# Kernel optimization log

Measured on AMD Instinct MI355X. Metric: run time of the kernel, lower is better.

Reference implementation:

```python
import jax, jax.numpy as jnp
import numpy as np

EPS = 1e-5

def layer_norm(h, g, b):
    mu = h.mean(axis=-1, keepdims=True)
    var = jnp.mean((h - mu) ** 2, axis=-1, keepdims=True)
    return (h - mu) * jax.lax.rsqrt(var + EPS) * g + b

def setup_inputs() -> dict:
    key = jax.random.key(0)
    B, J, D, Ae, A, H, EH, LAT = 32, 16384, 32, 16, 4096, 128, 256, 32
    ks = jax.random.split(key, 12)
    in_dim = 1 + D + Ae  # 49
    inp = {
        "x": jax.random.normal(ks[0], (B, J), dtype=jnp.float32),
        "mask": jax.random.randint(ks[1], (B, J), 0, 2, dtype=jnp.int32),
        "atse_index": jax.random.randint(ks[2], (J,), 0, A, dtype=jnp.int32),
        "feature_embedding": jax.random.normal(ks[3], (J, D), dtype=jnp.float32),
        "atse_embedding": jax.random.normal(ks[4], (A, Ae), dtype=jnp.float32),
        # h_layer: Linear(in_dim->H) + LN + ReLU + Linear(H->D) + LN + ReLU
        "hW1": jax.random.normal(ks[5], (in_dim, H), dtype=jnp.float32) / np.sqrt(in_dim),
        "hb1": jnp.zeros((H,), jnp.float32),
        "hg1": jnp.ones((H,), jnp.float32),
        "hB1": jnp.zeros((H,), jnp.float32),
        "hW2": jax.random.normal(ks[6], (H, D), dtype=jnp.float32) / np.sqrt(H),
        "hb2": jnp.zeros((D,), jnp.float32),
        "hg2": jnp.ones((D,), jnp.float32),
        "hB2": jnp.zeros((D,), jnp.float32),
        # encoder_mlp (FCLayers, 2 layers, LayerNorm + ReLU each): D->EH->2*LAT
        "eW1": jax.random.normal(ks[7], (D, EH), dtype=jnp.float32) / np.sqrt(D),
        "eb1": jnp.zeros((EH,), jnp.float32),
        "eg1": jnp.ones((EH,), jnp.float32),
        "eB1": jnp.zeros((EH,), jnp.float32),
        "eW2": jax.random.normal(ks[8], (EH, 2 * LAT), dtype=jnp.float32) / np.sqrt(EH),
        "eb2": jnp.zeros((2 * LAT,), jnp.float32),
        "eg2": jnp.ones((2 * LAT,), jnp.float32),
        "eB2": jnp.zeros((2 * LAT,), jnp.float32),
    }
    return inp

def reference(x, mask, atse_index, feature_embedding, atse_embedding,
              hW1, hb1, hg1, hB1, hW2, hb2, hg2, hB2,
              eW1, eb1, eg1, eB1, eW2, eb2, eg2, eB2):
    B, J = x.shape
    Ae_per_j = atse_embedding[atse_index]  # [J, Ae] gather
    # h_in per (b, j): [psi | F_j | E_atse(j)] -> [B, J, 1+D+Ae]
    h_in = jnp.concatenate([
        x[:, :, None],
        jnp.broadcast_to(feature_embedding[None], (B,) + feature_embedding.shape),
        jnp.broadcast_to(Ae_per_j[None], (B,) + Ae_per_j.shape),
    ], axis=-1)
    h = jax.nn.relu(layer_norm(h_in @ hW1 + hb1, hg1, hB1))   # [B, J, H]
    h = jax.nn.relu(layer_norm(h @ hW2 + hb2, hg2, hB2))      # [B, J, D]
    m = mask.astype(h.dtype)                                   # [B, J]
    pooled = jnp.einsum('bj,bjd->bd', m, h)                    # masked sum pool
    cnt = m.sum(axis=-1, keepdims=True)
    c = pooled / jnp.maximum(cnt, 1.0)                         # mean; zero rows stay zero
    e = jax.nn.relu(layer_norm(c @ eW1 + eb1, eg1, eB1))
    ml = jax.nn.relu(layer_norm(e @ eW2 + eb2, eg2, eB2))      # [B, 2*latent]
    mu, logvar = jnp.split(ml, 2, axis=-1)
    return mu, logvar
```

## Files before the change

kernel.cpp:

```cpp
#include <hip/hip_runtime.h>
#include <hip/hip_bf16.h>

#define JTOT  16384
#define BATCH 32
#define DD    32
#define AE    16
#define HH    128
#define EHD   256
#define LATD  32
#define NBLK  512
#define EPSV  1e-5f

typedef __attribute__((ext_vector_type(8))) short short8;
typedef __attribute__((ext_vector_type(4))) float f32x4;

#define OFF_BASE 0
#define OFF_XS   4224
#define OFF_MS   5280
#define OFF_W0   6336
#define OFF_G1   6464
#define OFF_B1   6592
#define OFF_S0   6720
#define OFF_S1   6752
#define OFF_C1   6784
#define OFF_MW   6816
#define LDS_FLOATS 6848

__device__ __forceinline__ unsigned pk2(float lo, float hi) {
    float2 f; f.x = lo; f.y = hi;
    __hip_bfloat162 h = __float22bfloat162_rn(f);
    unsigned u; __builtin_memcpy(&u, &h, 4);
    return u;
}

__device__ __forceinline__ float aelem(float base_, float wv, float gv, float Bv,
                                       float xr, float rsr, float ccr) {
    float v = fmaf(xr, wv, base_);
    float t = fmaf(v, rsr, ccr);
    return fmaxf(fmaf(t, gv, Bv), 0.f);
}

__global__ __launch_bounds__(256, 2) void k_rows(
    const float* __restrict__ x, const int* __restrict__ mask,
    const int* __restrict__ aidx, const float* __restrict__ F,
    const float* __restrict__ AeE, const float* __restrict__ hW1,
    const float* __restrict__ hb1, const float* __restrict__ hg1,
    const float* __restrict__ hB1, const float* __restrict__ hW2,
    const float* __restrict__ hb2, const float* __restrict__ hg2,
    const float* __restrict__ hB2, float* __restrict__ partial)
{
    __shared__ float smem[LDS_FLOATS];
    const int tid = threadIdx.x;
    const int j0  = blockIdx.x * 32;

    float* BASEp = smem + OFF_BASE;
    float* XSp   = smem + OFF_XS;
    float* MSp   = smem + OFF_MS;
    float* W0p   = smem + OFF_W0;
    float* G1p   = smem + OFF_G1;
    float* B1p   = smem + OFF_B1;
    float* S0p   = smem + OFF_S0;
    float* S1p   = smem + OFF_S1;
    float* C1p   = smem + OFF_C1;
    float* MWp   = smem + OFF_MW;

    for (int o = tid; o < 1024; o += 256) {
        int b = o >> 5, jj = o & 31;
        XSp[b * 33 + jj] = x[b * JTOT + j0 + jj];
        MSp[b * 33 + jj] = (float)mask[b * JTOT + j0 + jj];
    }
    if (tid < HH) { W0p[tid] = hW1[tid]; G1p[tid] = hg1[tid]; B1p[tid] = hB1[tid]; }

    {
        const int kk = tid & 127;
        const int jh = tid >> 7;
        float w[48];
        #pragma unroll
        for (int i = 0; i < 48; ++i) w[i] = hW1[(1 + i) * HH + kk];
        const float hb1v = hb1[kk];
        #pragma unroll 2
        for (int r = 0; r < 16; ++r) {
            int jj = __builtin_amdgcn_readfirstlane(2 * r + jh);
            int j  = j0 + jj;
            const float4* Fj = (const float4*)(F + j * DD);
            const float4* Aj = (const float4*)(AeE + aidx[j] * AE);
            float acc = hb1v;
            #pragma unroll
            for (int i4 = 0; i4 < 8; ++i4) {
                float4 f = Fj[i4];
                acc = fmaf(f.x, w[i4 * 4 + 0], acc);
                acc = fmaf(f.y, w[i4 * 4 + 1], acc);
                acc = fmaf(f.z, w[i4 * 4 + 2], acc);
                acc = fmaf(f.w, w[i4 * 4 + 3], acc);
            }
            #pragma unroll
            for (int i4 = 0; i4 < 4; ++i4) {
                float4 a = Aj[i4];
                acc = fmaf(a.x, w[32 + i4 * 4 + 0], acc);
                acc = fmaf(a.y, w[32 + i4 * 4 + 1], acc);
                acc = fmaf(a.z, w[32 + i4 * 4 + 2], acc);
                acc = fmaf(a.w, w[32 + i4 * 4 + 3], acc);
            }
            BASEp[jj * 132 + kk] = acc;
        }
    }
    __syncthreads();

    {
        const int jj = tid >> 3, p = tid & 7;
        const float* bp = BASEp + jj * 132 + p * 16;
        const float* wp = W0p + p * 16;
        float s0 = 0.f, s1 = 0.f, c1 = 0.f;
        #pragma unroll
        for (int i = 0; i < 16; ++i) {
            float v = bp[i], wv = wp[i];
            s0 += v; s1 = fmaf(v, v, s1); c1 = fmaf(v, wv, c1);
        }
        #pragma unroll
        for (int m = 1; m < 8; m <<= 1) {
            s0 += __shfl_xor(s0, m); s1 += __shfl_xor(s1, m); c1 += __shfl_xor(c1, m);
        }
        if (p == 0) {
            S0p[jj] = s0 * (1.f / HH);
            S1p[jj] = s1 * (1.f / HH);
            C1p[jj] = c1 * (1.f / HH);
        }
    }
    if (tid < 64) {
        float a = W0p[tid], b = W0p[64 + tid];
        float s = a + b, qq = fmaf(a, a, b * b);
        #pragma unroll
        for (int m = 1; m < 64; m <<= 1) { s += __shfl_xor(s, m); qq += __shfl_xor(qq, m); }
        if (tid == 0) { MWp[0] = s * (1.f / HH); MWp[1] = qq * (1.f / HH); }
    }
    __syncthreads();

    const int lane = tid & 63;
    const int n = lane & 15, q = lane >> 4;

    short8 Bf[4][2];
    #pragma unroll
    for (int s = 0; s < 4; ++s)
        #pragma unroll
        for (int cb = 0; cb < 2; ++cb) {
            union { short8 v; unsigned u[4]; } t;
            #pragma unroll
            for (int p2 = 0; p2 < 4; ++p2) {
                int k0 = 32 * s + 8 * q + 2 * p2;
                float lo = hW2[(k0    ) * DD + cb * 16 + n];
                float hi = hW2[(k0 + 1) * DD + cb * 16 + n];
                t.u[p2] = pk2(lo, hi);
            }
            Bf[s][cb] = t.v;
        }

    float hb2v[2], g2v[2], B2v[2];
    #pragma unroll
    for (int cb = 0; cb < 2; ++cb) {
        hb2v[cb] = hb2[cb * 16 + n];
        g2v[cb]  = hg2[cb * 16 + n];
        B2v[cb]  = hB2[cb * 16 + n];
    }
    const float mw0v = MWp[0], sw0v = MWp[1];

    f32x4 pool[2][2];
    #pragma unroll
    for (int R = 0; R < 2; ++R)
        #pragma unroll
        for (int cb = 0; cb < 2; ++cb)
            pool[R][cb] = (f32x4){0.f, 0.f, 0.f, 0.f};

    const int wslot = tid >> 6;
    #pragma unroll 1
    for (int jl = 0; jl < 8; ++jl) {
        const int jj = wslot * 8 + jl;
        const float x0 = XSp[n * 33 + jj];
        const float x1 = XSp[(16 + n) * 33 + jj];
        const float S0 = S0p[jj], S1 = S1p[jj], C1 = C1p[jj];

        float mu0 = fmaf(x0, mw0v, S0);
        float e0  = fmaf(x0 * x0, sw0v, fmaf(2.f * x0, C1, S1));
        float rs0 = rsqrtf(fmaxf(e0 - mu0 * mu0, 0.f) + EPSV);
        float cc0 = -mu0 * rs0;
        float mu1 = fmaf(x1, mw0v, S0);
        float e1  = fmaf(x1 * x1, sw0v, fmaf(2.f * x1, C1, S1));
        float rs1 = rsqrtf(fmaxf(e1 - mu1 * mu1, 0.f) + EPSV);
        float cc1 = -mu1 * rs1;

        f32x4 a00 = {0.f,0.f,0.f,0.f}, a01 = {0.f,0.f,0.f,0.f};
        f32x4 a10 = {0.f,0.f,0.f,0.f}, a11 = {0.f,0.f,0.f,0.f};

        #pragma unroll
        for (int s = 0; s < 4; ++s) {
            const float* bp = BASEp + jj * 132 + 32 * s + 8 * q;
            float4 ba = *(const float4*)bp;
            float4 bb = *(const float4*)(bp + 4);
            const float* wp = W0p + 32 * s + 8 * q;
            float4 wa = *(const float4*)wp;
            float4 wb = *(const float4*)(wp + 4);
            const float* gp = G1p + 32 * s + 8 * q;
            float4 ga = *(const float4*)gp;
            float4 gb = *(const float4*)(gp + 4);
            const float* Bp = B1p + 32 * s + 8 * q;
            float4 Ca = *(const float4*)Bp;
            float4 Cb2 = *(const float4*)(Bp + 4);

            union { short8 v; unsigned u[4]; } A0, A1;
            A0.u[0] = pk2(aelem(ba.x, wa.x, ga.x, Ca.x,  x0, rs0, cc0),
                          aelem(ba.y, wa.y, ga.y, Ca.y,  x0, rs0, cc0));
            A0.u[1] = pk2(aelem(ba.z, wa.z, ga.z, Ca.z,  x0, rs0, cc0),
                          aelem(ba.w, wa.w, ga.w, Ca.w,  x0, rs0, cc0));
            A0.u[2] = pk2(aelem(bb.x, wb.x, gb.x, Cb2.x, x0, rs0, cc0),
                          aelem(bb.y, wb.y, gb.y, Cb2.y, x0, rs0, cc0));
            A0.u[3] = pk2(aelem(bb.z, wb.z, gb.z, Cb2.z, x0, rs0, cc0),
                          aelem(bb.w, wb.w, gb.w, Cb2.w, x0, rs0, cc0));
            A1.u[0] = pk2(aelem(ba.x, wa.x, ga.x, Ca.x,  x1, rs1, cc1),
                          aelem(ba.y, wa.y, ga.y, Ca.y,  x1, rs1, cc1));
            A1.u[1] = pk2(aelem(ba.z, wa.z, ga.z, Ca.z,  x1, rs1, cc1),
                          aelem(ba.w, wa.w, ga.w, Ca.w,  x1, rs1, cc1));
            A1.u[2] = pk2(aelem(bb.x, wb.x, gb.x, Cb2.x, x1, rs1, cc1),
                          aelem(bb.y, wb.y, gb.y, Cb2.y, x1, rs1, cc1));
            A1.u[3] = pk2(aelem(bb.z, wb.z, gb.z, Cb2.z, x1, rs1, cc1),
                          aelem(bb.w, wb.w, gb.w, Cb2.w, x1, rs1, cc1));

            a00 = __builtin_amdgcn_mfma_f32_16x16x32_bf16(A0.v, Bf[s][0], a00, 0, 0, 0);
            a01 = __builtin_amdgcn_mfma_f32_16x16x32_bf16(A0.v, Bf[s][1], a01, 0, 0, 0);
            a10 = __builtin_amdgcn_mfma_f32_16x16x32_bf16(A1.v, Bf[s][0], a10, 0, 0, 0);
            a11 = __builtin_amdgcn_mfma_f32_16x16x32_bf16(A1.v, Bf[s][1], a11, 0, 0, 0);
        }

        #pragma unroll
        for (int r = 0; r < 4; ++r) {
            float t0 = a00[r] + hb2v[0];
            float t1 = a01[r] + hb2v[1];
            float s  = t0 + t1, ss = fmaf(t0, t0, t1 * t1);
            #pragma unroll
            for (int m = 1; m < 16; m <<= 1) { s += __shfl_xor(s, m); ss += __shfl_xor(ss, m); }
            float mu  = s * (1.f / DD);
            float var = ss * (1.f / DD) - mu * mu;
            float rs  = rsqrtf(fmaxf(var, 0.f) + EPSV);
            float cc  = -mu * rs;
            float mv  = MSp[(q * 4 + r) * 33 + jj];
            pool[0][0][r] = fmaf(fmaxf(fmaf(fmaf(t0, rs, cc), g2v[0], B2v[0]), 0.f), mv, pool[0][0][r]);
            pool[0][1][r] = fmaf(fmaxf(fmaf(fmaf(t1, rs, cc), g2v[1], B2v[1]), 0.f), mv, pool[0][1][r]);

            float u0 = a10[r] + hb2v[0];
            float u1 = a11[r] + hb2v[1];
            float s2 = u0 + u1, ss2 = fmaf(u0, u0, u1 * u1);
            #pragma unroll
            for (int m = 1; m < 16; m <<= 1) { s2 += __shfl_xor(s2, m); ss2 += __shfl_xor(ss2, m); }
            float mu2  = s2 * (1.f / DD);
            float var2 = ss2 * (1.f / DD) - mu2 * mu2;
            float rsB  = rsqrtf(fmaxf(var2, 0.f) + EPSV);
            float ccB  = -mu2 * rsB;
            float mv1  = MSp[(16 + q * 4 + r) * 33 + jj];
            pool[1][0][r] = fmaf(fmaxf(fmaf(fmaf(u0, rsB, ccB), g2v[0], B2v[0]), 0.f), mv1, pool[1][0][r]);
            pool[1][1][r] = fmaf(fmaxf(fmaf(fmaf(u1, rsB, ccB), g2v[1], B2v[1]), 0.f), mv1, pool[1][1][r]);
        }
    }

    __syncthreads();
    #pragma unroll
    for (int R = 0; R < 2; ++R)
        #pragma unroll
        for (int cb = 0; cb < 2; ++cb)
            #pragma unroll
            for (int r = 0; r < 4; ++r) {
                int b = R * 16 + q * 4 + r, d = cb * 16 + n;
                smem[wslot * 1024 + b * 32 + d] = pool[R][cb][r];
            }
    __syncthreads();
    for (int o = tid; o < 1024; o += 256) {
        float sv = smem[o] + smem[1024 + o] + smem[2048 + o] + smem[3072 + o];
        partial[blockIdx.x * 1024 + o] = sv;
    }
}

__global__ __launch_bounds__(256) void k_final(
    const float* __restrict__ partial, const int* __restrict__ mask,
    const float* __restrict__ eW1,
    const float* __restrict__ eb1, const float* __restrict__ eg1,
    const float* __restrict__ eB1,
    const float* __restrict__ eW2,
    const float* __restrict__ eb2, const float* __restrict__ eg2,
    const float* __restrict__ eB2,
    float* __restrict__ out, int nblk)
{
    const int b   = blockIdx.x;
    const int tid = threadIdx.x;

    __shared__ float red[8 * DD];
    __shared__ float cw[4], ws1[4], ws2[4];
    __shared__ float cS[DD];
    __shared__ float eS[EHD];

    {
        const int d  = tid & 31;
        const int c8 = tid >> 5;
        float s = 0.f;
        for (int blk = c8; blk < nblk; blk += 8)
            s += partial[(blk * BATCH + b) * DD + d];
        red[c8 * DD + d] = s;
    }
    float cs = 0.f;
    for (int i = tid; i < JTOT; i += 256) cs += (float)mask[b * JTOT + i];
    #pragma unroll
    for (int m = 1; m < 64; m <<= 1) cs += __shfl_xor(cs, m);
    if ((tid & 63) == 0) cw[tid >> 6] = cs;
    __syncthreads();

    if (tid < DD) {
        float c = 0.f;
        #pragma unroll
        for (int i = 0; i < 8; ++i) c += red[i * DD + tid];
        float cnt = cw[0] + cw[1] + cw[2] + cw[3];
        cS[tid] = c / fmaxf(cnt, 1.f);
    }
    __syncthreads();

    float e = eb1[tid];
    #pragma unroll
    for (int i = 0; i < DD; ++i) e = fmaf(cS[i], eW1[i * EHD + tid], e);

    float sum = e, ssq = e * e;
    #pragma unroll
    for (int m = 1; m < 64; m <<= 1) { sum += __shfl_xor(sum, m); ssq += __shfl_xor(ssq, m); }
    if ((tid & 63) == 0) { ws1[tid >> 6] = sum; ws2[tid >> 6] = ssq; }
    __syncthreads();
    float S1 = ws1[0] + ws1[1] + ws1[2] + ws1[3];
    float S2 = ws2[0] + ws2[1] + ws2[2] + ws2[3];
    float mu = S1 * (1.f / EHD);
    float var = S2 * (1.f / EHD) - mu * mu;
    float rs = rsqrtf(var + EPSV);
    eS[tid] = fmaxf(fmaf((e - mu) * rs, eg1[tid], eB1[tid]), 0.f);
    __syncthreads();

    if (tid < 2 * LATD) {
        float ml = eb2[tid];
        #pragma unroll 8
        for (int i = 0; i < EHD; ++i) ml = fmaf(eS[i], eW2[i * (2 * LATD) + tid], ml);
        float s = ml, qv = ml * ml;
        #pragma unroll
        for (int m = 1; m < 64; m <<= 1) { s += __shfl_xor(s, m); qv += __shfl_xor(qv, m); }
        float mu2 = s * (1.f / (2 * LATD));
        float var2 = qv * (1.f / (2 * LATD)) - mu2 * mu2;
        float rs2 = rsqrtf(var2 + EPSV);
        float v = fmaxf(fmaf((ml - mu2) * rs2, eg2[tid], eB2[tid]), 0.f);
        if (tid < LATD) out[b * LATD + tid] = v;
        else            out[BATCH * LATD + b * LATD + (tid - LATD)] = v;
    }
}

extern "C" void kernel_launch(void* const* d_in, const int* in_sizes, int n_in,
                              void* d_out, int out_size, void* d_ws, size_t ws_size,
                              hipStream_t stream) {
    const float* x    = (const float*)d_in[0];
    const int*   mask = (const int*)  d_in[1];
    const int*   aidx = (const int*)  d_in[2];
    const float* F    = (const float*)d_in[3];
    const float* AeE  = (const float*)d_in[4];
    const float* hW1  = (const float*)d_in[5];
    const float* hb1  = (const float*)d_in[6];
    const float* hg1  = (const float*)d_in[7];
    const float* hB1  = (const float*)d_in[8];
    const float* hW2  = (const float*)d_in[9];
    const float* hb2  = (const float*)d_in[10];
    const float* hg2  = (const float*)d_in[11];
    const float* hB2  = (const float*)d_in[12];
    const float* eW1  = (const float*)d_in[13];
    const float* eb1  = (const float*)d_in[14];
    const float* eg1  = (const float*)d_in[15];
    const float* eB1  = (const float*)d_in[16];
    const float* eW2  = (const float*)d_in[17];
    const float* eb2  = (const float*)d_in[18];
    const float* eg2  = (const float*)d_in[19];
    const float* eB2  = (const float*)d_in[20];
    float* out = (float*)d_out;

    float* partial = (float*)d_ws;

    k_rows<<<dim3(NBLK), dim3(256), 0, stream>>>(
        x, mask, aidx, F, AeE, hW1, hb1, hg1, hB1, hW2, hb2, hg2, hB2, partial);
    k_final<<<dim3(BATCH), dim3(256), 0, stream>>>(
        partial, mask, eW1, eb1, eg1, eB1, eW2, eb2, eg2, eB2, out, NBLK);
}
```

Measured before the change: 183.4 us.

## Halve j-tile per block, transpose MFMA operands, pack FMAs, widen final reduction

The row kernel now handles 16 j values per block instead of 32, doubling the grid to 1024 blocks and raising the launch-bounds occupancy hint from 2 to 4 with a smaller LDS footprint. The first-layer projection and the layer-norm activation are computed with two-wide float vectors so the compiler can emit packed FMA instructions. The MFMA operands are swapped so that W2 is the A operand, which puts d along rows and cuts the per-row LN2 reduction down to two cross-lane shuffles. The final kernel uses 1024 threads and int4 mask loads to reduce the larger number of partial sums faster. The trade-off is twice as many partials to reduce and more redundant weight loads per block.

New measurement: 216.1 us. 1.18x slower.

```diff
diff --git a/kernel.cpp b/kernel.cpp
--- a/kernel.cpp
+++ b/kernel.cpp
@@ -8,23 +8,43 @@
 #define HH    128
 #define EHD   256
 #define LATD  32
-#define NBLK  512
+#define JT    16
+#define NBLK  1024
 #define EPSV  1e-5f
 
 typedef __attribute__((ext_vector_type(8))) short short8;
 typedef __attribute__((ext_vector_type(4))) float f32x4;
+typedef __attribute__((ext_vector_type(2))) float v2f;
+
+static __device__ __forceinline__ v2f mk2(float a, float b) {
+    v2f r; r.x = a; r.y = b; return r;
+}
+static __device__ __forceinline__ v2f FMA2(v2f a, v2f b, v2f c) {
+#if __has_builtin(__builtin_elementwise_fma)
+    return __builtin_elementwise_fma(a, b, c);
+#else
+    v2f r; r.x = fmaf(a.x, b.x, c.x); r.y = fmaf(a.y, b.y, c.y); return r;
+#endif
+}
+static __device__ __forceinline__ v2f MAX2(v2f a, v2f b) {
+#if __has_builtin(__builtin_elementwise_max)
+    return __builtin_elementwise_max(a, b);
+#else
+    v2f r; r.x = fmaxf(a.x, b.x); r.y = fmaxf(a.y, b.y); return r;
+#endif
+}
 
 #define OFF_BASE 0
-#define OFF_XS   4224
-#define OFF_MS   5280
-#define OFF_W0   6336
-#define OFF_G1   6464
-#define OFF_B1   6592
-#define OFF_S0   6720
-#define OFF_S1   6752
-#define OFF_C1   6784
-#define OFF_MW   6816
-#define LDS_FLOATS 6848
+#define OFF_XS   2112
+#define OFF_MS   2656
+#define OFF_W0   3200
+#define OFF_G1   3328
+#define OFF_B1   3456
+#define OFF_S0   3584
+#define OFF_S1   3600
+#define OFF_C1   3616
+#define OFF_MW   3632
+#define LDS_FLOATS 4224
 
 __device__ __forceinline__ unsigned pk2(float lo, float hi) {
     float2 f; f.x = lo; f.y = hi;
@@ -33,14 +53,16 @@
     return u;
 }
 
-__device__ __forceinline__ float aelem(float base_, float wv, float gv, float Bv,
-                                       float xr, float rsr, float ccr) {
-    float v = fmaf(xr, wv, base_);
-    float t = fmaf(v, rsr, ccr);
-    return fmaxf(fmaf(t, gv, Bv), 0.f);
-}
-
-__global__ __launch_bounds__(256, 2) void k_rows(
+__device__ __forceinline__ unsigned pke(v2f b, v2f w, v2f g, v2f Bl,
+                                        float x, float rs, float cc) {
+    v2f u = FMA2(mk2(x, x), w, b);
+    v2f t = FMA2(u, mk2(rs, rs), mk2(cc, cc));
+    v2f h = FMA2(t, g, Bl);
+    h = MAX2(h, mk2(0.f, 0.f));
+    return pk2(h.x, h.y);
+}
+
+__global__ __launch_bounds__(256, 4) void k_rows(
     const float* __restrict__ x, const int* __restrict__ mask,
     const int* __restrict__ aidx, const float* __restrict__ F,
     const float* __restrict__ AeE, const float* __restrict__ hW1,
@@ -51,7 +73,7 @@
 {
     __shared__ float smem[LDS_FLOATS];
     const int tid = threadIdx.x;
-    const int j0  = blockIdx.x * 32;
+    const int j0  = blockIdx.x * JT;
 
     float* BASEp = smem + OFF_BASE;
     float* XSp   = smem + OFF_XS;
@@ -64,10 +86,10 @@
     float* C1p   = smem + OFF_C1;
     float* MWp   = smem + OFF_MW;
 
-    for (int o = tid; o < 1024; o += 256) {
-        int b = o >> 5, jj = o & 31;
-        XSp[b * 33 + jj] = x[b * JTOT + j0 + jj];
-        MSp[b * 33 + jj] = (float)mask[b * JTOT + j0 + jj];
+    for (int o = tid; o < 512; o += 256) {
+        int b = o >> 4, jj = o & 15;
+        XSp[b * 17 + jj] = x[b * JTOT + j0 + jj];
+        MSp[b * 17 + jj] = (float)mask[b * JTOT + j0 + jj];
     }
     if (tid < HH) { W0p[tid] = hW1[tid]; G1p[tid] = hg1[tid]; B1p[tid] = hB1[tid]; }
 
@@ -78,46 +100,48 @@
         #pragma unroll
         for (int i = 0; i < 48; ++i) w[i] = hW1[(1 + i) * HH + kk];
         const float hb1v = hb1[kk];
-        #pragma unroll 2
-        for (int r = 0; r < 16; ++r) {
-            int jj = __builtin_amdgcn_readfirstlane(2 * r + jh);
-            int j  = j0 + jj;
-            const float4* Fj = (const float4*)(F + j * DD);
-            const float4* Aj = (const float4*)(AeE + aidx[j] * AE);
-            float acc = hb1v;
+        #pragma unroll
+        for (int pr = 0; pr < 4; ++pr) {
+            const int jja = 4 * pr + jh, jjb = jja + 2;
+            const float4* Fa = (const float4*)(F + (j0 + jja) * DD);
+            const float4* Fb = (const float4*)(F + (j0 + jjb) * DD);
+            const float4* Aa = (const float4*)(AeE + aidx[j0 + jja] * AE);
+            const float4* Ab = (const float4*)(AeE + aidx[j0 + jjb] * AE);
+            v2f acc = mk2(hb1v, hb1v);
             #pragma unroll
             for (int i4 = 0; i4 < 8; ++i4) {
-                float4 f = Fj[i4];
-                acc = fmaf(f.x, w[i4 * 4 + 0], acc);
-                acc = fmaf(f.y, w[i4 * 4 + 1], acc);
-                acc = fmaf(f.z, w[i4 * 4 + 2], acc);
-                acc = fmaf(f.w, w[i4 * 4 + 3], acc);
+                float4 fa = Fa[i4], fb = Fb[i4];
+                acc = FMA2(mk2(fa.x, fb.x), mk2(w[i4*4+0], w[i4*4+0]), acc);
+                acc = FMA2(mk2(fa.y, fb.y), mk2(w[i4*4+1], w[i4*4+1]), acc);
+                acc = FMA2(mk2(fa.z, fb.z), mk2(w[i4*4+2], w[i4*4+2]), acc);
+                acc = FMA2(mk2(fa.w, fb.w), mk2(w[i4*4+3], w[i4*4+3]), acc);
             }
             #pragma unroll
             for (int i4 = 0; i4 < 4; ++i4) {
-                float4 a = Aj[i4];
-                acc = fmaf(a.x, w[32 + i4 * 4 + 0], acc);
-                acc = fmaf(a.y, w[32 + i4 * 4 + 1], acc);
-                acc = fmaf(a.z, w[32 + i4 * 4 + 2], acc);
-                acc = fmaf(a.w, w[32 + i4 * 4 + 3], acc);
-            }
-            BASEp[jj * 132 + kk] = acc;
+                float4 fa = Aa[i4], fb = Ab[i4];
+                acc = FMA2(mk2(fa.x, fb.x), mk2(w[32+i4*4+0], w[32+i4*4+0]), acc);
+                acc = FMA2(mk2(fa.y, fb.y), mk2(w[32+i4*4+1], w[32+i4*4+1]), acc);
+                acc = FMA2(mk2(fa.z, fb.z), mk2(w[32+i4*4+2], w[32+i4*4+2]), acc);
+                acc = FMA2(mk2(fa.w, fb.w), mk2(w[32+i4*4+3], w[32+i4*4+3]), acc);
+            }
+            BASEp[jja * 132 + kk] = acc.x;
+            BASEp[jjb * 132 + kk] = acc.y;
         }
     }
     __syncthreads();
 
     {
-        const int jj = tid >> 3, p = tid & 7;
-        const float* bp = BASEp + jj * 132 + p * 16;
-        const float* wp = W0p + p * 16;
+        const int jj = tid >> 4, p = tid & 15;
+        const float* bp = BASEp + jj * 132 + p * 8;
+        const float* wp = W0p + p * 8;
         float s0 = 0.f, s1 = 0.f, c1 = 0.f;
         #pragma unroll
-        for (int i = 0; i < 16; ++i) {
+        for (int i = 0; i < 8; ++i) {
             float v = bp[i], wv = wp[i];
             s0 += v; s1 = fmaf(v, v, s1); c1 = fmaf(v, wv, c1);
         }
         #pragma unroll
-        for (int m = 1; m < 8; m <<= 1) {
+        for (int m = 1; m < 16; m <<= 1) {
             s0 += __shfl_xor(s0, m); s1 += __shfl_xor(s1, m); c1 += __shfl_xor(c1, m);
         }
         if (p == 0) {
@@ -137,45 +161,47 @@
 
     const int lane = tid & 63;
     const int n = lane & 15, q = lane >> 4;
-
-    short8 Bf[4][2];
+    const int wslot = tid >> 6;
+
+    short8 Af[4][2];
     #pragma unroll
     for (int s = 0; s < 4; ++s)
         #pragma unroll
-        for (int cb = 0; cb < 2; ++cb) {
+        for (int dt = 0; dt < 2; ++dt) {
             union { short8 v; unsigned u[4]; } t;
             #pragma unroll
             for (int p2 = 0; p2 < 4; ++p2) {
                 int k0 = 32 * s + 8 * q + 2 * p2;
-                float lo = hW2[(k0    ) * DD + cb * 16 + n];
-                float hi = hW2[(k0 + 1) * DD + cb * 16 + n];
-                t.u[p2] = pk2(lo, hi);
-            }
-            Bf[s][cb] = t.v;
-        }
-
-    float hb2v[2], g2v[2], B2v[2];
+                t.u[p2] = pk2(hW2[(k0    ) * DD + dt * 16 + n],
+                              hW2[(k0 + 1) * DD + dt * 16 + n]);
+            }
+            Af[s][dt] = t.v;
+        }
+
+    float hb2v[8], g2v[8], B2v[8];
     #pragma unroll
-    for (int cb = 0; cb < 2; ++cb) {
-        hb2v[cb] = hb2[cb * 16 + n];
-        g2v[cb]  = hg2[cb * 16 + n];
-        B2v[cb]  = hB2[cb * 16 + n];
-    }
+    for (int dt = 0; dt < 2; ++dt)
+        #pragma unroll
+        for (int r = 0; r < 4; ++r) {
+            int d = dt * 16 + 4 * q + r;
+            hb2v[dt*4+r] = hb2[d]; g2v[dt*4+r] = hg2[d]; B2v[dt*4+r] = hB2[d];
+        }
     const float mw0v = MWp[0], sw0v = MWp[1];
 
     f32x4 pool[2][2];
     #pragma unroll
-    for (int R = 0; R < 2; ++R)
-        #pragma unroll
-        for (int cb = 0; cb < 2; ++cb)
-            pool[R][cb] = (f32x4){0.f, 0.f, 0.f, 0.f};
-
-    const int wslot = tid >> 6;
+    for (int dt = 0; dt < 2; ++dt)
+        #pragma unroll
+        for (int bt = 0; bt < 2; ++bt)
+            pool[dt][bt] = (f32x4){0.f, 0.f, 0.f, 0.f};
+
     #pragma unroll 1
-    for (int jl = 0; jl < 8; ++jl) {
-        const int jj = wslot * 8 + jl;
-        const float x0 = XSp[n * 33 + jj];
-        const float x1 = XSp[(16 + n) * 33 + jj];
+    for (int jl = 0; jl < 4; ++jl) {
+        const int jj = wslot * 4 + jl;
+        const float x0  = XSp[n * 17 + jj];
+        const float x1  = XSp[(16 + n) * 17 + jj];
+        const float mv0 = MSp[n * 17 + jj];
+        const float mv1 = MSp[(16 + n) * 17 + jj];
         const float S0 = S0p[jj], S1 = S1p[jj], C1 = C1p[jj];
 
         float mu0 = fmaf(x0, mw0v, S0);
@@ -187,96 +213,91 @@
         float rs1 = rsqrtf(fmaxf(e1 - mu1 * mu1, 0.f) + EPSV);
         float cc1 = -mu1 * rs1;
 
-        f32x4 a00 = {0.f,0.f,0.f,0.f}, a01 = {0.f,0.f,0.f,0.f};
-        f32x4 a10 = {0.f,0.f,0.f,0.f}, a11 = {0.f,0.f,0.f,0.f};
+        f32x4 Cacc[2][2];
+        Cacc[0][0] = (f32x4){0.f,0.f,0.f,0.f}; Cacc[0][1] = (f32x4){0.f,0.f,0.f,0.f};
+        Cacc[1][0] = (f32x4){0.f,0.f,0.f,0.f}; Cacc[1][1] = (f32x4){0.f,0.f,0.f,0.f};
 
         #pragma unroll
         for (int s = 0; s < 4; ++s) {
-            const float* bp = BASEp + jj * 132 + 32 * s + 8 * q;
-            float4 ba = *(const float4*)bp;
-            float4 bb = *(const float4*)(bp + 4);
-            const float* wp = W0p + 32 * s + 8 * q;
-            float4 wa = *(const float4*)wp;
-            float4 wb = *(const float4*)(wp + 4);
-            const float* gp = G1p + 32 * s + 8 * q;
-            float4 ga = *(const float4*)gp;
-            float4 gb = *(const float4*)(gp + 4);
-            const float* Bp = B1p + 32 * s + 8 * q;
-            float4 Ca = *(const float4*)Bp;
-            float4 Cb2 = *(const float4*)(Bp + 4);
-
-            union { short8 v; unsigned u[4]; } A0, A1;
-            A0.u[0] = pk2(aelem(ba.x, wa.x, ga.x, Ca.x,  x0, rs0, cc0),
-                          aelem(ba.y, wa.y, ga.y, Ca.y,  x0, rs0, cc0));
-            A0.u[1] = pk2(aelem(ba.z, wa.z, ga.z, Ca.z,  x0, rs0, cc0),
-                          aelem(ba.w, wa.w, ga.w, Ca.w,  x0, rs0, cc0));
-            A0.u[2] = pk2(aelem(bb.x, wb.x, gb.x, Cb2.x, x0, rs0, cc0),
-                          aelem(bb.y, wb.y, gb.y, Cb2.y, x0, rs0, cc0));
-            A0.u[3] = pk2(aelem(bb.z, wb.z, gb.z, Cb2.z, x0, rs0, cc0),
-                          aelem(bb.w, wb.w, gb.w, Cb2.w, x0, rs0, cc0));
-            A1.u[0] = pk2(aelem(ba.x, wa.x, ga.x, Ca.x,  x1, rs1, cc1),
-                          aelem(ba.y, wa.y, ga.y, Ca.y,  x1, rs1, cc1));
-            A1.u[1] = pk2(aelem(ba.z, wa.z, ga.z, Ca.z,  x1, rs1, cc1),
-                          aelem(ba.w, wa.w, ga.w, Ca.w,  x1, rs1, cc1));
-            A1.u[2] = pk2(aelem(bb.x, wb.x, gb.x, Cb2.x, x1, rs1, cc1),
-                          aelem(bb.y, wb.y, gb.y, Cb2.y, x1, rs1, cc1));
-            A1.u[3] = pk2(aelem(bb.z, wb.z, gb.z, Cb2.z, x1, rs1, cc1),
-                          aelem(bb.w, wb.w, gb.w, Cb2.w, x1, rs1, cc1));
-
-            a00 = __builtin_amdgcn_mfma_f32_16x16x32_bf16(A0.v, Bf[s][0], a00, 0, 0, 0);
-            a01 = __builtin_amdgcn_mfma_f32_16x16x32_bf16(A0.v, Bf[s][1], a01, 0, 0, 0);
-            a10 = __builtin_amdgcn_mfma_f32_16x16x32_bf16(A1.v, Bf[s][0], a10, 0, 0, 0);
-            a11 = __builtin_amdgcn_mfma_f32_16x16x32_bf16(A1.v, Bf[s][1], a11, 0, 0, 0);
-        }
-
-        #pragma unroll
-        for (int r = 0; r < 4; ++r) {
-            float t0 = a00[r] + hb2v[0];
-            float t1 = a01[r] + hb2v[1];
-            float s  = t0 + t1, ss = fmaf(t0, t0, t1 * t1);
-            #pragma unroll
-            for (int m = 1; m < 16; m <<= 1) { s += __shfl_xor(s, m); ss += __shfl_xor(ss, m); }
+            const int off = 32 * s + 8 * q;
+            const float* bp = BASEp + jj * 132 + off;
+            union { short8 v; unsigned u[4]; } B0, B1;
+            {
+                float4 ba = *(const float4*)bp;
+                float4 wa = *(const float4*)(W0p + off);
+                float4 ga = *(const float4*)(G1p + off);
+                float4 ca = *(const float4*)(B1p + off);
+                B0.u[0] = pke(mk2(ba.x,ba.y), mk2(wa.x,wa.y), mk2(ga.x,ga.y), mk2(ca.x,ca.y), x0, rs0, cc0);
+                B0.u[1] = pke(mk2(ba.z,ba.w), mk2(wa.z,wa.w), mk2(ga.z,ga.w), mk2(ca.z,ca.w), x0, rs0, cc0);
+                B1.u[0] = pke(mk2(ba.x,ba.y), mk2(wa.x,wa.y), mk2(ga.x,ga.y), mk2(ca.x,ca.y), x1, rs1, cc1);
+                B1.u[1] = pke(mk2(ba.z,ba.w), mk2(wa.z,wa.w), mk2(ga.z,ga.w), mk2(ca.z,ca.w), x1, rs1, cc1);
+            }
+            {
+                float4 bb = *(const float4*)(bp + 4);
+                float4 wb = *(const float4*)(W0p + off + 4);
+                float4 gb = *(const float4*)(G1p + off + 4);
+                float4 cb = *(const float4*)(B1p + off + 4);
+                B0.u[2] = pke(mk2(bb.x,bb.y), mk2(wb.x,wb.y), mk2(gb.x,gb.y), mk2(cb.x,cb.y), x0, rs0, cc0);
+                B0.u[3] = pke(mk2(bb.z,bb.w), mk2(wb.z,wb.w), mk2(gb.z,gb.w), mk2(cb.z,cb.w), x0, rs0, cc0);
+                B1.u[2] = pke(mk2(bb.x,bb.y), mk2(wb.x,wb.y), mk2(gb.x,gb.y), mk2(cb.x,cb.y), x1, rs1, cc1);
+                B1.u[3] = pke(mk2(bb.z,bb.w), mk2(wb.z,wb.w), mk2(gb.z,gb.w), mk2(cb.z,cb.w), x1, rs1, cc1);
+            }
+            Cacc[0][0] = __builtin_amdgcn_mfma_f32_16x16x32_bf16(Af[s][0], B0.v, Cacc[0][0], 0, 0, 0);
+            Cacc[0][1] = __builtin_amdgcn_mfma_f32_16x16x32_bf16(Af[s][0], B1.v, Cacc[0][1], 0, 0, 0);
+            Cacc[1][0] = __builtin_amdgcn_mfma_f32_16x16x32_bf16(Af[s][1], B0.v, Cacc[1][0], 0, 0, 0);
+            Cacc[1][1] = __builtin_amdgcn_mfma_f32_16x16x32_bf16(Af[s][1], B1.v, Cacc[1][1], 0, 0, 0);
+        }
+
+        #pragma unroll
+        for (int bt = 0; bt < 2; ++bt) {
+            float v[8];
+            float s = 0.f, ss = 0.f;
+            #pragma unroll
+            for (int dt = 0; dt < 2; ++dt)
+                #pragma unroll
+                for (int r = 0; r < 4; ++r) {
+                    float t = Cacc[dt][bt][r] + hb2v[dt*4+r];
+                    v[dt*4+r] = t;
+                    s += t; ss = fmaf(t, t, ss);
+                }
+            s  += __shfl_xor(s, 16);  s  += __shfl_xor(s, 32);
+            ss += __shfl_xor(ss, 16); ss += __shfl_xor(ss, 32);
             float mu  = s * (1.f / DD);
             float var = ss * (1.f / DD) - mu * mu;
             float rs  = rsqrtf(fmaxf(var, 0.f) + EPSV);
             float cc  = -mu * rs;
-            float mv  = MSp[(q * 4 + r) * 33 + jj];
-            pool[0][0][r] = fmaf(fmaxf(fmaf(fmaf(t0, rs, cc), g2v[0], B2v[0]), 0.f), mv, pool[0][0][r]);
-            pool[0][1][r] = fmaf(fmaxf(fmaf(fmaf(t1, rs, cc), g2v[1], B2v[1]), 0.f), mv, pool[0][1][r]);
-
-            float u0 = a10[r] + hb2v[0];
-            float u1 = a11[r] + hb2v[1];
-            float s2 = u0 + u1, ss2 = fmaf(u0, u0, u1 * u1);
-            #pragma unroll
-            for (int m = 1; m < 16; m <<= 1) { s2 += __shfl_xor(s2, m); ss2 += __shfl_xor(ss2, m); }
-            float mu2  = s2 * (1.f / DD);
-            float var2 = ss2 * (1.f / DD) - mu2 * mu2;
-            float rsB  = rsqrtf(fmaxf(var2, 0.f) + EPSV);
-            float ccB  = -mu2 * rsB;
-            float mv1  = MSp[(16 + q * 4 + r) * 33 + jj];
-            pool[1][0][r] = fmaf(fmaxf(fmaf(fmaf(u0, rsB, ccB), g2v[0], B2v[0]), 0.f), mv1, pool[1][0][r]);
-            pool[1][1][r] = fmaf(fmaxf(fmaf(fmaf(u1, rsB, ccB), g2v[1], B2v[1]), 0.f), mv1, pool[1][1][r]);
+            float mv  = bt ? mv1 : mv0;
+            #pragma unroll
+            for (int dt = 0; dt < 2; ++dt)
+                #pragma unroll
+                for (int r = 0; r < 4; ++r) {
+                    float t = fmaf(v[dt*4+r], rs, cc);
+                    float h = fmaxf(fmaf(t, g2v[dt*4+r], B2v[dt*4+r]), 0.f);
+                    pool[dt][bt][r] = fmaf(h, mv, pool[dt][bt][r]);
+                }
         }
     }
 
     __syncthreads();
     #pragma unroll
-    for (int R = 0; R < 2; ++R)
-        #pragma unroll
-        for (int cb = 0; cb < 2; ++cb)
+    for (int dt = 0; dt < 2; ++dt)
+        #pragma unroll
+        for (int bt = 0; bt < 2; ++bt)
             #pragma unroll
             for (int r = 0; r < 4; ++r) {
-                int b = R * 16 + q * 4 + r, d = cb * 16 + n;
-                smem[wslot * 1024 + b * 32 + d] = pool[R][cb][r];
+                int d = dt * 16 + 4 * q + r, b = bt * 16 + n;
+                smem[wslot * 1056 + b * 33 + d] = pool[dt][bt][r];
             }
     __syncthreads();
     for (int o = tid; o < 1024; o += 256) {
-        float sv = smem[o] + smem[1024 + o] + smem[2048 + o] + smem[3072 + o];
+        int b = o >> 5, d = o & 31;
+        int a = b * 33 + d;
+        float sv = smem[a] + smem[1056 + a] + smem[2112 + a] + smem[3168 + a];
         partial[blockIdx.x * 1024 + o] = sv;
     }
 }
 
-__global__ __launch_bounds__(256) void k_final(
+__global__ __launch_bounds__(1024) void k_final(
     const float* __restrict__ partial, const int* __restrict__ mask,
     const float* __restrict__ eW1,
     const float* __restrict__ eb1, const float* __restrict__ eg1,
@@ -289,50 +310,61 @@
     const int b   = blockIdx.x;
     const int tid = threadIdx.x;
 
-    __shared__ float red[8 * DD];
-    __shared__ float cw[4], ws1[4], ws2[4];
+    __shared__ float red[32 * 32];
+    __shared__ float cw[16], ws1[4], ws2[4];
     __shared__ float cS[DD];
     __shared__ float eS[EHD];
 
     {
-        const int d  = tid & 31;
-        const int c8 = tid >> 5;
+        const int c = tid >> 5, d = tid & 31;
         float s = 0.f;
-        for (int blk = c8; blk < nblk; blk += 8)
-            s += partial[(blk * BATCH + b) * DD + d];
-        red[c8 * DD + d] = s;
-    }
-    float cs = 0.f;
-    for (int i = tid; i < JTOT; i += 256) cs += (float)mask[b * JTOT + i];
-    #pragma unroll
-    for (int m = 1; m < 64; m <<= 1) cs += __shfl_xor(cs, m);
-    if ((tid & 63) == 0) cw[tid >> 6] = cs;
+        for (int i = c; i < nblk; i += 32)
+            s += partial[i * 1024 + b * 32 + d];
+        red[c * 32 + d] = s;
+    }
+    {
+        const int4* m4 = (const int4*)(mask + b * JTOT);
+        float cs = 0.f;
+        for (int i = tid; i < JTOT / 4; i += 1024) {
+            int4 v = m4[i];
+            cs += (float)(v.x + v.y + v.z + v.w);
+        }
+        #pragma unroll
+        for (int m = 1; m < 64; m <<= 1) cs += __shfl_xor(cs, m);
+        if ((tid & 63) == 0) cw[tid >> 6] = cs;
+    }
     __syncthreads();
 
     if (tid < DD) {
         float c = 0.f;
         #pragma unroll
-        for (int i = 0; i < 8; ++i) c += red[i * DD + tid];
-        float cnt = cw[0] + cw[1] + cw[2] + cw[3];
+        for (int i = 0; i < 32; ++i) c += red[i * 32 + tid];
+        float cnt = 0.f;
+        #pragma unroll
+        for (int i = 0; i < 16; ++i) cnt += cw[i];
         cS[tid] = c / fmaxf(cnt, 1.f);
     }
     __syncthreads();
 
-    float e = eb1[tid];
-    #pragma unroll
-    for (int i = 0; i < DD; ++i) e = fmaf(cS[i], eW1[i * EHD + tid], e);
-
-    float sum = e, ssq = e * e;
-    #pragma unroll
-    for (int m = 1; m < 64; m <<= 1) { sum += __shfl_xor(sum, m); ssq += __shfl_xor(ssq, m); }
-    if ((tid & 63) == 0) { ws1[tid >> 6] = sum; ws2[tid >> 6] = ssq; }
-    __syncthreads();
-    float S1 = ws1[0] + ws1[1] + ws1[2] + ws1[3];
-    float S2 = ws2[0] + ws2[1] + ws2[2] + ws2[3];
-    float mu = S1 * (1.f / EHD);
-    float var = S2 * (1.f / EHD) - mu * mu;
-    float rs = rsqrtf(var + EPSV);
-    eS[tid] = fmaxf(fmaf((e - mu) * rs, eg1[tid], eB1[tid]), 0.f);
+    if (tid < EHD) {
+        float e = eb1[tid];
+        #pragma unroll
+        for (int i = 0; i < DD; ++i) e = fmaf(cS[i], eW1[i * EHD + tid], e);
+        float sum = e, ssq = e * e;
+        #pragma unroll
+        for (int m = 1; m < 64; m <<= 1) { sum += __shfl_xor(sum, m); ssq += __shfl_xor(ssq, m); }
+        if ((tid & 63) == 0) { ws1[tid >> 6] = sum; ws2[tid >> 6] = ssq; }
+        eS[tid] = e;
+    }
+    __syncthreads();
+    if (tid < EHD) {
+        float S1 = ws1[0] + ws1[1] + ws1[2] + ws1[3];
+        float S2 = ws2[0] + ws2[1] + ws2[2] + ws2[3];
+        float mu = S1 * (1.f / EHD);
+        float var = S2 * (1.f / EHD) - mu * mu;
+        float rs = rsqrtf(var + EPSV);
+        eS[tid] = fmaxf(fmaf((eS[tid] - mu) * rs, eg1[tid], eB1[tid]), 0.f);
+    }
     __syncthreads();
 
     if (tid < 2 * LATD) {
@@ -381,6 +413,6 @@
 
     k_rows<<<dim3(NBLK), dim3(256), 0, stream>>>(
         x, mask, aidx, F, AeE, hW1, hb1, hg1, hB1, hW2, hb2, hg2, hB2, partial);
-    k_final<<<dim3(BATCH), dim3(256), 0, stream>>>(
+    k_final<<<dim3(BATCH), dim3(1024), 0, stream>>>(
         partial, mask, eW1, eb1, eg1, eB1, eW2, eb2, eg2, eB2, out, NBLK);
 }
```
